# Optimization experiments

Hardware: AMD Instinct MI355X
Metric: run time of the kernel (lower is better)

Reference implementation:

```python
import jax, jax.numpy as jnp
import numpy as np

LN_EPS = 1e-5


def _ln(x, g, b):
    m = jnp.mean(x, axis=-1, keepdims=True)
    v = jnp.mean((x - m) ** 2, axis=-1, keepdims=True)
    return (x - m) / jnp.sqrt(v + LN_EPS) * g + b


def setup_inputs() -> dict:
    key = jax.random.key(0)
    ks = jax.random.split(key, 8)
    B, N, S, D, T = 16, 64, 2048, 1024, 768

    def xavier(k, shape):
        fan_in, fan_out = shape
        lim = (6.0 / (fan_in + fan_out)) ** 0.5
        return jax.random.uniform(k, shape, minval=-lim, maxval=lim, dtype=jnp.float32)

    return {
        "prev_states": jax.random.normal(ks[0], (B, N, D), dtype=jnp.float32),
        "input_tokens": jax.random.normal(ks[1], (B, S, T), dtype=jnp.float32),
        # input_projection (token_dim -> state_dim)
        "W_proj": xavier(ks[2], (T, D)),
        "b_proj": jnp.zeros((D,), jnp.float32),
        # three LayerNorms
        "g_state": jnp.ones((D,), jnp.float32), "beta_state": jnp.zeros((D,), jnp.float32),
        "g_input": jnp.ones((D,), jnp.float32), "beta_input": jnp.zeros((D,), jnp.float32),
        "g_out": jnp.ones((D,), jnp.float32), "beta_out": jnp.zeros((D,), jnp.float32),
        # GRU gates (2D -> D); update-gate bias initialized to -1 as in the module
        "W_u": xavier(ks[3], (2 * D, D)), "b_u": jnp.full((D,), -1.0, jnp.float32),
        "W_r": xavier(ks[4], (2 * D, D)), "b_r": jnp.zeros((D,), jnp.float32),
        "W_n": xavier(ks[5], (2 * D, D)), "b_n": jnp.zeros((D,), jnp.float32),
    }


def reference(prev_states, input_tokens, W_proj, b_proj,
              g_state, beta_state, g_input, beta_input, g_out, beta_out,
              W_u, b_u, W_r, b_r, W_n, b_n):
    D = prev_states.shape[-1]
    # project tokens to state dim: (B,S,D)
    tok = input_tokens @ W_proj + b_proj
    # attention routing (routing_weights=None path)
    scores = jnp.einsum('bnd,bsd->bns', prev_states, tok) / jnp.sqrt(jnp.float32(D))
    attn = jax.nn.softmax(scores, axis=-1)
    routed = jnp.einsum('bns,bsd->bnd', attn, tok)  # (B,N,D)
    # GRU-style gated update, vectorized over the num_states axis
    ps_n = _ln(prev_states, g_state, beta_state)
    in_n = _ln(routed, g_input, beta_input)
    concat = jnp.concatenate([ps_n, in_n], axis=-1)  # (B,N,2D)
    u = jax.nn.sigmoid(concat @ W_u + b_u)
    r = jax.nn.sigmoid(concat @ W_r + b_r)
    reset_in = jnp.concatenate([r * ps_n, in_n], axis=-1)
    cand = jnp.tanh(reset_in @ W_n + b_n)  # dropout is identity in eval
    new_state = (1.0 - u) * prev_states + u * cand
    return _ln(new_state, g_out, beta_out)
```

## Files before the change

kernel.cpp:

```cpp
#include <hip/hip_runtime.h>
#include <stdint.h>

typedef __attribute__((ext_vector_type(4))) float floatx4;
typedef __attribute__((ext_vector_type(8))) short shortx8;

#define LN_EPS 1e-5f

__device__ __forceinline__ unsigned short f2b(float f) {
  unsigned u = __builtin_bit_cast(unsigned, f);
  u = (u + 0x7FFFu + ((u >> 16) & 1u)) >> 16;
  return (unsigned short)u;
}
__device__ __forceinline__ float b2f(unsigned short h) {
  return __builtin_bit_cast(float, (unsigned)h << 16);
}

__device__ __forceinline__ void g2l16(const unsigned short* g, unsigned short* l) {
  __builtin_amdgcn_global_load_lds(
      (const __attribute__((address_space(1))) unsigned int*)g,
      (__attribute__((address_space(3))) unsigned int*)l, 16, 0, 0);
}

__device__ __forceinline__ float wave_sum(float v) {
#pragma unroll
  for (int o = 32; o; o >>= 1) v += __shfl_down(v, o, 64);
  return v;
}
__device__ __forceinline__ float block_sum(float v, float* s) {
  v = wave_sum(v);
  __syncthreads();
  if ((threadIdx.x & 63) == 0) s[threadIdx.x >> 6] = v;
  __syncthreads();
  return s[0] + s[1] + s[2] + s[3];
}

__global__ __launch_bounds__(256) void k_transpose_to_bf16(
    const float* __restrict__ in, unsigned short* __restrict__ out, int K, int N) {
  __shared__ float tile[32][33];
  const int k0 = blockIdx.x * 32, n0 = blockIdx.y * 32;
  const int tx = threadIdx.x & 31, ty = threadIdx.x >> 5;
#pragma unroll
  for (int i = 0; i < 32; i += 8)
    tile[ty + i][tx] = in[(long)(k0 + ty + i) * N + n0 + tx];
  __syncthreads();
#pragma unroll
  for (int i = 0; i < 32; i += 8)
    out[(long)(n0 + ty + i) * K + k0 + tx] = f2b(tile[tx][ty + i]);
}

__global__ __launch_bounds__(256) void k_transpose3(
    const float* __restrict__ Wu, const float* __restrict__ Wr,
    const float* __restrict__ Wn, unsigned short* __restrict__ Wtur,
    unsigned short* __restrict__ Wtn) {
  __shared__ float tile[32][33];
  const int which = blockIdx.z;
  const float* in = which == 0 ? Wu : (which == 1 ? Wr : Wn);
  unsigned short* out = which == 0 ? Wtur : (which == 1 ? Wtur + 1024 * 2048 : Wtn);
  const int K = 2048, N = 1024;
  const int k0 = blockIdx.x * 32, n0 = blockIdx.y * 32;
  const int tx = threadIdx.x & 31, ty = threadIdx.x >> 5;
#pragma unroll
  for (int i = 0; i < 32; i += 8)
    tile[ty + i][tx] = in[(long)(k0 + ty + i) * N + n0 + tx];
  __syncthreads();
#pragma unroll
  for (int i = 0; i < 32; i += 8)
    out[(long)(n0 + ty + i) * K + k0 + tx] = f2b(tile[tx][ty + i]);
}

__global__ __launch_bounds__(256) void k_cvt2(
    const float* __restrict__ prev, unsigned short* __restrict__ psb,
    const float* __restrict__ toks, unsigned short* __restrict__ tokb) {
  const long chunk = (long)blockIdx.x * 256 + threadIdx.x;
  const float* src;
  unsigned short* dst;
  long i;
  if (chunk < 262144) { src = prev; dst = psb; i = chunk * 4; }
  else { src = toks; dst = tokb; i = (chunk - 262144) * 4; }
  floatx4 v = *(const floatx4*)(src + i);
  unsigned short t4[4];
#pragma unroll
  for (int j = 0; j < 4; j++) t4[j] = f2b(v[j]);
  *(uint2*)(dst + i) = *(uint2*)t4;
}

__global__ __launch_bounds__(256) void k_proj128(
    const unsigned short* __restrict__ A, const unsigned short* __restrict__ Bt,
    const float* __restrict__ bias, unsigned short* __restrict__ C) {
  constexpr int K = 768;
  constexpr int N = 1024;
  __shared__ unsigned short As[128 * 64];
  __shared__ unsigned short Bs[128 * 64];
  const int tid = threadIdx.x;
  const int wave = tid >> 6, lane = tid & 63;
  const int id = blockIdx.x;
  const int m0 = (((id >> 6) << 3) + (id & 7)) * 128;
  const int n0 = ((id >> 3) & 7) * 128;
  const int wm = wave & 1, wn = wave >> 1;
  const int l16 = lane & 15, quad = lane >> 4;
  const int srow8 = lane >> 3;
  const int c8 = ((lane & 7) ^ srow8) * 8;

  const unsigned short* gA[4];
  const unsigned short* gB[4];
  unsigned short* lA[4];
  unsigned short* lB[4];
#pragma unroll
  for (int j = 0; j < 4; j++) {
    const int rb = wave * 32 + j * 8;
    gA[j] = A + (long)(m0 + rb + srow8) * K + c8;
    gB[j] = Bt + (long)(n0 + rb + srow8) * K + c8;
    lA[j] = &As[rb * 64];
    lB[j] = &Bs[rb * 64];
  }
  int offA[2][4], offB[2][4];
#pragma unroll
  for (int ks = 0; ks < 2; ks++)
#pragma unroll
    for (int i = 0; i < 4; i++) {
      int r = wm * 64 + i * 16 + l16;
      offA[ks][i] = r * 64 + (((ks * 4 + quad) ^ (r & 7)) * 8);
      r = wn * 64 + i * 16 + l16;
      offB[ks][i] = r * 64 + (((ks * 4 + quad) ^ (r & 7)) * 8);
    }

  floatx4 acc[4][4] = {};

  for (int k0 = 0; k0 < K; k0 += 64) {
#pragma unroll
    for (int j = 0; j < 4; j++) {
      g2l16(gA[j] + k0, lA[j]);
      g2l16(gB[j] + k0, lB[j]);
    }
    __syncthreads();
#pragma unroll
    for (int ks = 0; ks < 2; ks++) {
      shortx8 af[4], bf[4];
#pragma unroll
      for (int i = 0; i < 4; i++) af[i] = *(const shortx8*)&As[offA[ks][i]];
#pragma unroll
      for (int j = 0; j < 4; j++) bf[j] = *(const shortx8*)&Bs[offB[ks][j]];
#pragma unroll
      for (int i = 0; i < 4; i++)
#pragma unroll
        for (int j = 0; j < 4; j++)
          acc[i][j] = __builtin_amdgcn_mfma_f32_16x16x32_bf16(af[i], bf[j], acc[i][j], 0, 0, 0);
    }
    __syncthreads();
  }

#pragma unroll
  for (int i = 0; i < 4; i++)
#pragma unroll
    for (int j = 0; j < 4; j++) {
      const int rbase = m0 + wm * 64 + i * 16 + quad * 4;
      const int col = n0 + wn * 64 + j * 16 + l16;
      const float bval = bias[col];
#pragma unroll
      for (int r = 0; r < 4; r++)
        C[(long)(rbase + r) * N + col] = f2b(acc[i][j][r] + bval);
    }
}

__global__ __launch_bounds__(256) void k_gemm64(
    const unsigned short* __restrict__ A, long sAb, long sAk, int lda,
    const unsigned short* __restrict__ Bt, long sBb, long sBk, int ldb,
    int K, int nsplit,
    const float* __restrict__ bias, const float* __restrict__ bias2,
    float scale, int mode,
    void* __restrict__ out, int ldc, long sCb, long sCk,
    unsigned short* __restrict__ out2,
    const unsigned short* __restrict__ aux_psn,
    const float* __restrict__ aux_u, const float* __restrict__ aux_prev) {
  __shared__ unsigned short As[64 * 64];
  __shared__ unsigned short Bs[64 * 64];
  const int tid = threadIdx.x;
  const int wave = tid >> 6, lane = tid & 63;
  const int z = blockIdx.z;
  const int b = (nsplit == 2) ? (z >> 1) : z;
  const int kc = (nsplit == 2) ? (z & 1) : 0;
  const int m0 = blockIdx.x * 64, n0 = blockIdx.y * 64;
  const int wm = wave & 1, wn = wave >> 1;
  const int l16 = lane & 15, quad = lane >> 4;
  const int srow8 = lane >> 3;
  const int c8 = ((lane & 7) ^ srow8) * 8;
  const unsigned short* Ab = A + (long)b * sAb + (long)kc * sAk;
  const unsigned short* Bb = Bt + (long)b * sBb + (long)kc * sBk;

  const unsigned short* gA[2];
  const unsigned short* gB[2];
  unsigned short* lA[2];
  unsigned short* lB[2];
#pragma unroll
  for (int j = 0; j < 2; j++) {
    const int rb = wave * 16 + j * 8;
    gA[j] = Ab + (long)(m0 + rb + srow8) * lda + c8;
    gB[j] = Bb + (long)(n0 + rb + srow8) * ldb + c8;
    lA[j] = &As[rb * 64];
    lB[j] = &Bs[rb * 64];
  }
  int offA[2][2], offB[2][2];
#pragma unroll
  for (int ks = 0; ks < 2; ks++)
#pragma unroll
    for (int i = 0; i < 2; i++) {
      int r = wm * 32 + i * 16 + l16;
      offA[ks][i] = r * 64 + (((ks * 4 + quad) ^ (r & 7)) * 8);
      r = wn * 32 + i * 16 + l16;
      offB[ks][i] = r * 64 + (((ks * 4 + quad) ^ (r & 7)) * 8);
    }

  floatx4 acc[2][2] = {};

  for (int k0 = 0; k0 < K; k0 += 64) {
#pragma unroll
    for (int j = 0; j < 2; j++) {
      g2l16(gA[j] + k0, lA[j]);
      g2l16(gB[j] + k0, lB[j]);
    }
    __syncthreads();
#pragma unroll
    for (int ks = 0; ks < 2; ks++) {
      shortx8 af[2], bf[2];
#pragma unroll
      for (int i = 0; i < 2; i++) af[i] = *(const shortx8*)&As[offA[ks][i]];
#pragma unroll
      for (int j = 0; j < 2; j++) bf[j] = *(const shortx8*)&Bs[offB[ks][j]];
#pragma unroll
      for (int i = 0; i < 2; i++)
#pragma unroll
        for (int j = 0; j < 2; j++)
          acc[i][j] = __builtin_amdgcn_mfma_f32_16x16x32_bf16(af[i], bf[j], acc[i][j], 0, 0, 0);
    }
    __syncthreads();
  }

#pragma unroll
  for (int i = 0; i < 2; i++)
#pragma unroll
    for (int j = 0; j < 2; j++) {
      const int rbase = m0 + wm * 32 + i * 16 + quad * 4;
      const int c = n0 + wn * 32 + j * 16 + l16;
      float bval = 0.0f;
      if (bias) bval = (mode == 5 && c >= 1024) ? bias2[c - 1024] : bias[c];
#pragma unroll
      for (int r = 0; r < 4; r++) {
        const int row = rbase + r;
        float v = acc[i][j][r] * scale + bval;
        const long cidx = (long)b * sCb + (long)kc * sCk + (long)row * ldc + c;
        if (mode == 0) {
          out2[cidx] = f2b(expf(v));
        } else if (mode == 3) {
          float cand = tanhf(v);
          float u = aux_u[(long)row * 1024 + c];
          float p = aux_prev[(long)row * 1024 + c];
          ((float*)out)[cidx] = (1.0f - u) * p + u * cand;
        } else {
          if (c < 1024) {
            ((float*)out)[(long)row * 1024 + c] = 1.0f / (1.0f + expf(-v));
          } else {
            const int cc = c - 1024;
            float rr = 1.0f / (1.0f + expf(-v));
            out2[(long)row * 2048 + cc] = f2b(rr * b2f(aux_psn[(long)row * 2048 + cc]));
          }
        }
      }
    }
}

__global__ __launch_bounds__(256) void k_routed_mfma(
    const unsigned short* __restrict__ attnb,
    const unsigned short* __restrict__ tok,
    float* __restrict__ parts) {
  __shared__ unsigned short As[64 * 40];
  __shared__ unsigned short Bs[32 * 66];
  const int kc = blockIdx.x, nt = blockIdx.y, b = blockIdx.z;
  const int tid = threadIdx.x;
  const int wave = tid >> 6, lane = tid & 63;
  const int wm = wave & 1, wn = wave >> 1;
  const int l16 = lane & 15, quad = lane >> 4;
  const int n0 = nt * 64;
  const long abase = (long)b * 131072 + (long)kc * 1024;
  const long tbase = ((long)b * 2048 + (long)kc * 1024) * 1024;
  const int srow = tid >> 2, skc = (tid & 3) * 8;
  const int bk = tid >> 3, bd = (tid & 7) * 8;

  floatx4 acc[2][2] = {};

  for (int k0 = 0; k0 < 1024; k0 += 32) {
    *(uint4*)&As[srow * 40 + skc] =
        *(const uint4*)(attnb + abase + (long)srow * 2048 + k0 + skc);
    {
      uint4 v = *(const uint4*)(tok + tbase + (long)(k0 + bk) * 1024 + n0 + bd);
      const unsigned* pv = (const unsigned*)&v;
      unsigned short* dst = &Bs[bk * 66 + bd];
#pragma unroll
      for (int w2 = 0; w2 < 4; w2++) *(unsigned*)(dst + w2 * 2) = pv[w2];
    }
    __syncthreads();

    shortx8 a0 = *(const shortx8*)&As[(wm * 32 + 0  + l16) * 40 + quad * 8];
    shortx8 a1 = *(const shortx8*)&As[(wm * 32 + 16 + l16) * 40 + quad * 8];
    shortx8 b0, b1;
#pragma unroll
    for (int j = 0; j < 8; j++) {
      b0[j] = *(const short*)&Bs[(quad * 8 + j) * 66 + wn * 32 + l16];
      b1[j] = *(const short*)&Bs[(quad * 8 + j) * 66 + wn * 32 + 16 + l16];
    }
    acc[0][0] = __builtin_amdgcn_mfma_f32_16x16x32_bf16(a0, b0, acc[0][0], 0, 0, 0);
    acc[0][1] = __builtin_amdgcn_mfma_f32_16x16x32_bf16(a0, b1, acc[0][1], 0, 0, 0);
    acc[1][0] = __builtin_amdgcn_mfma_f32_16x16x32_bf16(a1, b0, acc[1][0], 0, 0, 0);
    acc[1][1] = __builtin_amdgcn_mfma_f32_16x16x32_bf16(a1, b1, acc[1][1], 0, 0, 0);
    __syncthreads();
  }

#pragma unroll
  for (int im = 0; im < 2; im++)
#pragma unroll
    for (int in_ = 0; in_ < 2; in_++) {
      const int rbase = wm * 32 + im * 16 + quad * 4;
      const int c = n0 + wn * 32 + in_ * 16 + l16;
#pragma unroll
      for (int r = 0; r < 4; r++)
        parts[(long)kc * 1048576 + ((long)b * 64 + rbase + r) * 1024 + c] =
            acc[im][in_][r];
    }
}

__global__ __launch_bounds__(256) void k_ln2(
    const float* __restrict__ prev, const float* __restrict__ parts,
    const float* __restrict__ g_st, const float* __restrict__ be_st,
    const float* __restrict__ g_in, const float* __restrict__ be_in,
    unsigned short* __restrict__ conc, unsigned short* __restrict__ candA) {
  __shared__ float scr[4];
  const long r = blockIdx.x & 1023;
  const bool second = blockIdx.x >= 1024;
  const int t = threadIdx.x;
  floatx4 v;
  const float *g, *be;
  if (!second) {
    v = *(const floatx4*)(prev + r * 1024 + t * 4);
    g = g_st; be = be_st;
  } else {
    v = *(const floatx4*)(parts + r * 1024 + t * 4);
    v += *(const floatx4*)(parts + 1048576 + r * 1024 + t * 4);
    g = g_in; be = be_in;
  }
  float s1 = v[0] + v[1] + v[2] + v[3];
  float s2 = v[0] * v[0] + v[1] * v[1] + v[2] * v[2] + v[3] * v[3];
  s1 = block_sum(s1, scr);
  s2 = block_sum(s2, scr);
  const float mean = s1 * (1.0f / 1024.0f);
  const float var = s2 * (1.0f / 1024.0f) - mean * mean;
  const float rstd = rsqrtf(var + LN_EPS);
#pragma unroll
  for (int i = 0; i < 4; i++) {
    const int d = t * 4 + i;
    const float y = (v[i] - mean) * rstd * g[d] + be[d];
    const unsigned short h = f2b(y);
    if (!second) {
      conc[r * 2048 + d] = h;
    } else {
      conc[r * 2048 + 1024 + d] = h;
      candA[r * 2048 + 1024 + d] = h;
    }
  }
}

__global__ __launch_bounds__(256) void k_ln_out(
    const float* __restrict__ in, const float* __restrict__ g,
    const float* __restrict__ be, float* __restrict__ out) {
  __shared__ float scr[4];
  const long r = blockIdx.x;
  const int t = threadIdx.x;
  floatx4 v = *(const floatx4*)(in + r * 1024 + t * 4);
  float s1 = v[0] + v[1] + v[2] + v[3];
  float s2 = v[0] * v[0] + v[1] * v[1] + v[2] * v[2] + v[3] * v[3];
  s1 = block_sum(s1, scr);
  s2 = block_sum(s2, scr);
  const float mean = s1 * (1.0f / 1024.0f);
  const float var = s2 * (1.0f / 1024.0f) - mean * mean;
  const float rstd = rsqrtf(var + LN_EPS);
  floatx4 o;
#pragma unroll
  for (int i = 0; i < 4; i++) {
    const int d = t * 4 + i;
    o[i] = (v[i] - mean) * rstd * g[d] + be[d];
  }
  *(floatx4*)(out + r * 1024 + t * 4) = o;
}

extern "C" void kernel_launch(void* const* d_in, const int* in_sizes, int n_in,
                              void* d_out, int out_size, void* d_ws, size_t ws_size,
                              hipStream_t stream) {
  (void)in_sizes; (void)n_in; (void)out_size; (void)ws_size;
  const float* prev  = (const float*)d_in[0];
  const float* toks  = (const float*)d_in[1];
  const float* Wp    = (const float*)d_in[2];
  const float* bp    = (const float*)d_in[3];
  const float* g_st  = (const float*)d_in[4];
  const float* be_st = (const float*)d_in[5];
  const float* g_in  = (const float*)d_in[6];
  const float* be_in = (const float*)d_in[7];
  const float* g_o   = (const float*)d_in[8];
  const float* be_o  = (const float*)d_in[9];
  const float* Wu    = (const float*)d_in[10];
  const float* bu    = (const float*)d_in[11];
  const float* Wr    = (const float*)d_in[12];
  const float* br    = (const float*)d_in[13];
  const float* Wn    = (const float*)d_in[14];
  const float* bn    = (const float*)d_in[15];
  float* out = (float*)d_out;

  char* ws = (char*)d_ws;
  unsigned short* tok   = (unsigned short*)ws; ws += 67108864;
  unsigned short* Wtp   = (unsigned short*)ws; ws += 1572864;
  unsigned short* psb   = (unsigned short*)ws; ws += 2097152;
  char* U = ws;
  unsigned short* tokb  = (unsigned short*)U;
  char* u = U;
  unsigned short* attnb = (unsigned short*)u; u += 4194304;
  float*          parts = (float*)u;          u += 8388608;
  unsigned short* conc  = (unsigned short*)u; u += 4194304;
  unsigned short* candA = (unsigned short*)u; u += 4194304;
  float*          ubuf  = (float*)u;          u += 4194304;
  float*          ns    = (float*)u;          u += 4194304;
  unsigned short* Wtur  = (unsigned short*)u; u += 8388608;
  unsigned short* Wtn   = (unsigned short*)u; u += 4194304;

  const dim3 blk(256);

  k_cvt2<<<dim3(25600), blk, 0, stream>>>(prev, psb, toks, tokb);
  k_transpose_to_bf16<<<dim3(24, 32), blk, 0, stream>>>(Wp, Wtp, 768, 1024);
  k_proj128<<<dim3(2048), blk, 0, stream>>>(tokb, Wtp, bp, tok);
  k_transpose3<<<dim3(64, 32, 3), blk, 0, stream>>>(Wu, Wr, Wn, Wtur, Wtn);
  k_gemm64<<<dim3(1, 32, 16), blk, 0, stream>>>(
      psb, 65536L, 0L, 1024, tok, 2097152L, 0L, 1024, 1024, 1,
      nullptr, nullptr, 0.03125f, 0,
      nullptr, 2048, 131072L, 0L, attnb, nullptr, nullptr, nullptr);
  k_routed_mfma<<<dim3(2, 16, 16), blk, 0, stream>>>(attnb, tok, parts);
  k_ln2<<<dim3(2048), blk, 0, stream>>>(prev, parts, g_st, be_st, g_in, be_in,
                                        conc, candA);
  k_gemm64<<<dim3(16, 32, 1), blk, 0, stream>>>(
      conc, 0L, 0L, 2048, Wtur, 0L, 0L, 2048, 2048, 1,
      bu, br, 1.0f, 5,
      (void*)ubuf, 1024, 0L, 0L, candA, conc, nullptr, nullptr);
  k_gemm64<<<dim3(16, 16, 1), blk, 0, stream>>>(
      candA, 0L, 0L, 2048, Wtn, 0L, 0L, 2048, 2048, 1,
      bn, nullptr, 1.0f, 3,
      (void*)ns, 1024, 0L, 0L, nullptr, nullptr, ubuf, prev);
  k_ln_out<<<dim3(1024), blk, 0, stream>>>(ns, g_o, be_o, out);
}
```

Before: 367.6 us.

## Reassociate projection: fold W_proj into queries and apply after routing

Result: faster. 340.8 us (-7.3%).

```diff
diff --git a/kernel.cpp b/kernel.cpp
--- a/kernel.cpp
+++ b/kernel.cpp
@@ -68,98 +68,22 @@
     out[(long)(n0 + ty + i) * K + k0 + tx] = f2b(tile[tx][ty + i]);
 }
 
-__global__ __launch_bounds__(256) void k_cvt2(
+__global__ __launch_bounds__(256) void k_cvt3(
     const float* __restrict__ prev, unsigned short* __restrict__ psb,
-    const float* __restrict__ toks, unsigned short* __restrict__ tokb) {
+    const float* __restrict__ toks, unsigned short* __restrict__ tokb,
+    const float* __restrict__ wp, unsigned short* __restrict__ wpb) {
   const long chunk = (long)blockIdx.x * 256 + threadIdx.x;
   const float* src;
   unsigned short* dst;
   long i;
   if (chunk < 262144) { src = prev; dst = psb; i = chunk * 4; }
-  else { src = toks; dst = tokb; i = (chunk - 262144) * 4; }
+  else if (chunk < 6553600) { src = toks; dst = tokb; i = (chunk - 262144) * 4; }
+  else { src = wp; dst = wpb; i = (chunk - 6553600) * 4; }
   floatx4 v = *(const floatx4*)(src + i);
   unsigned short t4[4];
 #pragma unroll
   for (int j = 0; j < 4; j++) t4[j] = f2b(v[j]);
   *(uint2*)(dst + i) = *(uint2*)t4;
-}
-
-__global__ __launch_bounds__(256) void k_proj128(
-    const unsigned short* __restrict__ A, const unsigned short* __restrict__ Bt,
-    const float* __restrict__ bias, unsigned short* __restrict__ C) {
-  constexpr int K = 768;
-  constexpr int N = 1024;
-  __shared__ unsigned short As[128 * 64];
-  __shared__ unsigned short Bs[128 * 64];
-  const int tid = threadIdx.x;
-  const int wave = tid >> 6, lane = tid & 63;
-  const int id = blockIdx.x;
-  const int m0 = (((id >> 6) << 3) + (id & 7)) * 128;
-  const int n0 = ((id >> 3) & 7) * 128;
-  const int wm = wave & 1, wn = wave >> 1;
-  const int l16 = lane & 15, quad = lane >> 4;
-  const int srow8 = lane >> 3;
-  const int c8 = ((lane & 7) ^ srow8) * 8;
-
-  const unsigned short* gA[4];
-  const unsigned short* gB[4];
-  unsigned short* lA[4];
-  unsigned short* lB[4];
-#pragma unroll
-  for (int j = 0; j < 4; j++) {
-    const int rb = wave * 32 + j * 8;
-    gA[j] = A + (long)(m0 + rb + srow8) * K + c8;
-    gB[j] = Bt + (long)(n0 + rb + srow8) * K + c8;
-    lA[j] = &As[rb * 64];
-    lB[j] = &Bs[rb * 64];
-  }
-  int offA[2][4], offB[2][4];
-#pragma unroll
-  for (int ks = 0; ks < 2; ks++)
-#pragma unroll
-    for (int i = 0; i < 4; i++) {
-      int r = wm * 64 + i * 16 + l16;
-      offA[ks][i] = r * 64 + (((ks * 4 + quad) ^ (r & 7)) * 8);
-      r = wn * 64 + i * 16 + l16;
-      offB[ks][i] = r * 64 + (((ks * 4 + quad) ^ (r & 7)) * 8);
-    }
-
-  floatx4 acc[4][4] = {};
-
-  for (int k0 = 0; k0 < K; k0 += 64) {
-#pragma unroll
-    for (int j = 0; j < 4; j++) {
-      g2l16(gA[j] + k0, lA[j]);
-      g2l16(gB[j] + k0, lB[j]);
-    }
-    __syncthreads();
-#pragma unroll
-    for (int ks = 0; ks < 2; ks++) {
-      shortx8 af[4], bf[4];
-#pragma unroll
-      for (int i = 0; i < 4; i++) af[i] = *(const shortx8*)&As[offA[ks][i]];
-#pragma unroll
-      for (int j = 0; j < 4; j++) bf[j] = *(const shortx8*)&Bs[offB[ks][j]];
-#pragma unroll
-      for (int i = 0; i < 4; i++)
-#pragma unroll
-        for (int j = 0; j < 4; j++)
-          acc[i][j] = __builtin_amdgcn_mfma_f32_16x16x32_bf16(af[i], bf[j], acc[i][j], 0, 0, 0);
-    }
-    __syncthreads();
-  }
-
-#pragma unroll
-  for (int i = 0; i < 4; i++)
-#pragma unroll
-    for (int j = 0; j < 4; j++) {
-      const int rbase = m0 + wm * 64 + i * 16 + quad * 4;
-      const int col = n0 + wn * 64 + j * 16 + l16;
-      const float bval = bias[col];
-#pragma unroll
-      for (int r = 0; r < 4; r++)
-        C[(long)(rbase + r) * N + col] = f2b(acc[i][j][r] + bval);
-    }
 }
 
 __global__ __launch_bounds__(256) void k_gemm64(
@@ -250,11 +174,15 @@
         const long cidx = (long)b * sCb + (long)kc * sCk + (long)row * ldc + c;
         if (mode == 0) {
           out2[cidx] = f2b(expf(v));
+        } else if (mode == 1) {
+          out2[cidx] = f2b(v);
         } else if (mode == 3) {
           float cand = tanhf(v);
           float u = aux_u[(long)row * 1024 + c];
           float p = aux_prev[(long)row * 1024 + c];
           ((float*)out)[cidx] = (1.0f - u) * p + u * cand;
+        } else if (mode == 6) {
+          ((float*)out)[cidx] = v + aux_u[row] * bias2[c];
         } else {
           if (c < 1024) {
             ((float*)out)[(long)row * 1024 + c] = 1.0f / (1.0f + expf(-v));
@@ -281,7 +209,7 @@
   const int l16 = lane & 15, quad = lane >> 4;
   const int n0 = nt * 64;
   const long abase = (long)b * 131072 + (long)kc * 1024;
-  const long tbase = ((long)b * 2048 + (long)kc * 1024) * 1024;
+  const long tbase = ((long)b * 2048 + (long)kc * 1024) * 768;
   const int srow = tid >> 2, skc = (tid & 3) * 8;
   const int bk = tid >> 3, bd = (tid & 7) * 8;
 
@@ -291,7 +219,7 @@
     *(uint4*)&As[srow * 40 + skc] =
         *(const uint4*)(attnb + abase + (long)srow * 2048 + k0 + skc);
     {
-      uint4 v = *(const uint4*)(tok + tbase + (long)(k0 + bk) * 1024 + n0 + bd);
+      uint4 v = *(const uint4*)(tok + tbase + (long)(k0 + bk) * 768 + n0 + bd);
       const unsigned* pv = (const unsigned*)&v;
       unsigned short* dst = &Bs[bk * 66 + bd];
 #pragma unroll
@@ -322,13 +250,38 @@
       const int c = n0 + wn * 32 + in_ * 16 + l16;
 #pragma unroll
       for (int r = 0; r < 4; r++)
-        parts[(long)kc * 1048576 + ((long)b * 64 + rbase + r) * 1024 + c] =
+        parts[(long)kc * 786432 + ((long)b * 64 + rbase + r) * 768 + c] =
             acc[im][in_][r];
     }
 }
 
+__global__ __launch_bounds__(256) void k_rowsum(
+    const unsigned short* __restrict__ w, float* __restrict__ rs) {
+  __shared__ float scr[4];
+  const long r = blockIdx.x;
+  const int t = threadIdx.x;
+  uint4 v = *(const uint4*)(w + r * 2048 + t * 8);
+  const unsigned short* h = (const unsigned short*)&v;
+  float s = 0.0f;
+#pragma unroll
+  for (int i = 0; i < 8; i++) s += b2f(h[i]);
+  s = block_sum(s, scr);
+  if (t == 0) rs[r] = s;
+}
+
+__global__ __launch_bounds__(256) void k_sumcvt(
+    const float* __restrict__ parts, unsigned short* __restrict__ out) {
+  const long i = ((long)blockIdx.x * 256 + threadIdx.x) * 4;
+  floatx4 v = *(const floatx4*)(parts + i);
+  floatx4 w = *(const floatx4*)(parts + 786432 + i);
+  unsigned short t4[4];
+#pragma unroll
+  for (int j = 0; j < 4; j++) t4[j] = f2b(v[j] + w[j]);
+  *(uint2*)(out + i) = *(uint2*)t4;
+}
+
 __global__ __launch_bounds__(256) void k_ln2(
-    const float* __restrict__ prev, const float* __restrict__ parts,
+    const float* __restrict__ prev, const float* __restrict__ routed,
     const float* __restrict__ g_st, const float* __restrict__ be_st,
     const float* __restrict__ g_in, const float* __restrict__ be_in,
     unsigned short* __restrict__ conc, unsigned short* __restrict__ candA) {
@@ -342,8 +295,7 @@
     v = *(const floatx4*)(prev + r * 1024 + t * 4);
     g = g_st; be = be_st;
   } else {
-    v = *(const floatx4*)(parts + r * 1024 + t * 4);
-    v += *(const floatx4*)(parts + 1048576 + r * 1024 + t * 4);
+    v = *(const floatx4*)(routed + r * 1024 + t * 4);
     g = g_in; be = be_in;
   }
   float s1 = v[0] + v[1] + v[2] + v[3];
@@ -413,33 +365,44 @@
   float* out = (float*)d_out;
 
   char* ws = (char*)d_ws;
-  unsigned short* tok   = (unsigned short*)ws; ws += 67108864;
+  unsigned short* tokb  = (unsigned short*)ws; ws += 50331648;
+  unsigned short* psb   = (unsigned short*)ws; ws += 2097152;
+  unsigned short* Wpb   = (unsigned short*)ws; ws += 1572864;
   unsigned short* Wtp   = (unsigned short*)ws; ws += 1572864;
-  unsigned short* psb   = (unsigned short*)ws; ws += 2097152;
-  char* U = ws;
-  unsigned short* tokb  = (unsigned short*)U;
-  char* u = U;
-  unsigned short* attnb = (unsigned short*)u; u += 4194304;
-  float*          parts = (float*)u;          u += 8388608;
-  unsigned short* conc  = (unsigned short*)u; u += 4194304;
-  unsigned short* candA = (unsigned short*)u; u += 4194304;
-  float*          ubuf  = (float*)u;          u += 4194304;
-  float*          ns    = (float*)u;          u += 4194304;
-  unsigned short* Wtur  = (unsigned short*)u; u += 8388608;
-  unsigned short* Wtn   = (unsigned short*)u; u += 4194304;
+  unsigned short* pwb   = (unsigned short*)ws; ws += 1572864;
+  unsigned short* attnb = (unsigned short*)ws; ws += 4194304;
+  float*          rowsum= (float*)ws;          ws += 4096;
+  float*          parts = (float*)ws;          ws += 6291456;
+  unsigned short* rwb   = (unsigned short*)ws; ws += 1572864;
+  float*          routed= (float*)ws;          ws += 4194304;
+  unsigned short* conc  = (unsigned short*)ws; ws += 4194304;
+  unsigned short* candA = (unsigned short*)ws; ws += 4194304;
+  float*          ubuf  = (float*)ws;          ws += 4194304;
+  float*          ns    = (float*)ws;          ws += 4194304;
+  unsigned short* Wtur  = (unsigned short*)ws; ws += 8388608;
+  unsigned short* Wtn   = (unsigned short*)ws; ws += 4194304;
 
   const dim3 blk(256);
 
-  k_cvt2<<<dim3(25600), blk, 0, stream>>>(prev, psb, toks, tokb);
+  k_cvt3<<<dim3(26368), blk, 0, stream>>>(prev, psb, toks, tokb, Wp, Wpb);
   k_transpose_to_bf16<<<dim3(24, 32), blk, 0, stream>>>(Wp, Wtp, 768, 1024);
-  k_proj128<<<dim3(2048), blk, 0, stream>>>(tokb, Wtp, bp, tok);
   k_transpose3<<<dim3(64, 32, 3), blk, 0, stream>>>(Wu, Wr, Wn, Wtur, Wtn);
+  k_gemm64<<<dim3(16, 12, 1), blk, 0, stream>>>(
+      psb, 0L, 0L, 1024, Wpb, 0L, 0L, 1024, 1024, 1,
+      nullptr, nullptr, 1.0f, 1,
+      nullptr, 768, 0L, 0L, pwb, nullptr, nullptr, nullptr);
   k_gemm64<<<dim3(1, 32, 16), blk, 0, stream>>>(
-      psb, 65536L, 0L, 1024, tok, 2097152L, 0L, 1024, 1024, 1,
+      pwb, 49152L, 0L, 768, tokb, 1572864L, 0L, 768, 768, 1,
       nullptr, nullptr, 0.03125f, 0,
       nullptr, 2048, 131072L, 0L, attnb, nullptr, nullptr, nullptr);
-  k_routed_mfma<<<dim3(2, 16, 16), blk, 0, stream>>>(attnb, tok, parts);
-  k_ln2<<<dim3(2048), blk, 0, stream>>>(prev, parts, g_st, be_st, g_in, be_in,
+  k_rowsum<<<dim3(1024), blk, 0, stream>>>(attnb, rowsum);
+  k_routed_mfma<<<dim3(2, 12, 16), blk, 0, stream>>>(attnb, tokb, parts);
+  k_sumcvt<<<dim3(768), blk, 0, stream>>>(parts, rwb);
+  k_gemm64<<<dim3(16, 16, 1), blk, 0, stream>>>(
+      rwb, 0L, 0L, 768, Wtp, 0L, 0L, 768, 768, 1,
+      nullptr, bp, 1.0f, 6,
+      (void*)routed, 1024, 0L, 0L, nullptr, nullptr, rowsum, nullptr);
+  k_ln2<<<dim3(2048), blk, 0, stream>>>(prev, routed, g_st, be_st, g_in, be_in,
                                         conc, candA);
   k_gemm64<<<dim3(16, 32, 1), blk, 0, stream>>>(
       conc, 0L, 0L, 2048, Wtur, 0L, 0L, 2048, 2048, 1,
```
